# Performance work log

Measured on AMD Instinct MI355X. Metric: run time of the kernel, lower is better.

## Reference

```python
import jax, jax.numpy as jnp
import numpy as np

D_MODEL = 2048
NUM_HEADS = 16
D_K = D_MODEL // NUM_HEADS
LORA_R = 8
LORA_ALPHA = 16
SCALING = LORA_ALPHA / LORA_R  # 2.0
B, S = 2, 2048


def setup_inputs() -> dict:
    key = jax.random.key(0)
    ks = jax.random.split(key, 17)
    s = 1.0 / np.sqrt(D_MODEL)
    d = {"x": jax.random.normal(ks[0], (B, S, D_MODEL), jnp.float32)}
    i = 1
    for name in ("q", "k", "v", "o"):
        d[f"W{name}"] = jax.random.uniform(ks[i], (D_MODEL, D_MODEL), jnp.float32, -s, s); i += 1
        d[f"b{name}"] = jax.random.uniform(ks[i], (D_MODEL,), jnp.float32, -s, s); i += 1
        d[f"A{name}"] = jax.random.uniform(ks[i], (LORA_R, D_MODEL), jnp.float32, -s, s); i += 1
        # lora_B is zero-initialized in the module, but use small random so grads flow meaningfully
        d[f"B{name}"] = jax.random.normal(ks[i], (D_MODEL, LORA_R), jnp.float32) * 0.01; i += 1
    return d


def _lora_linear(x, W, b, A, Bm):
    # F.linear(x, W, b) + (x @ A.T @ B.T) * scaling
    return x @ W.T + b + ((x @ A.T) @ Bm.T) * SCALING


def reference(x, Wq, bq, Aq, Bq, Wk, bk, Ak, Bk, Wv, bv, Av, Bv, Wo, bo, Ao, Bo):
    batch = x.shape[0]
    q = _lora_linear(x, Wq, bq, Aq, Bq)
    k = _lora_linear(x, Wk, bk, Ak, Bk)
    v = _lora_linear(x, Wv, bv, Av, Bv)
    # [B, S, H, Dk] -> [B, H, S, Dk]
    q = q.reshape(batch, -1, NUM_HEADS, D_K).transpose(0, 2, 1, 3)
    k = k.reshape(batch, -1, NUM_HEADS, D_K).transpose(0, 2, 1, 3)
    v = v.reshape(batch, -1, NUM_HEADS, D_K).transpose(0, 2, 1, 3)
    scores = jnp.einsum("bhqd,bhkd->bhqk", q, k) / jnp.sqrt(jnp.float32(D_K))
    attn = jax.nn.softmax(scores, axis=-1)
    context = jnp.einsum("bhqk,bhkd->bhqd", attn, v)
    context = context.transpose(0, 2, 1, 3).reshape(batch, -1, D_MODEL)
    return _lora_linear(context, Wo, bo, Ao, Bo)
```

## Files before the change

kernel.cpp:

```cpp
#include <hip/hip_runtime.h>
#include <stdint.h>

typedef unsigned short u16;
typedef unsigned int   u32;
typedef __bf16  bf16x8 __attribute__((ext_vector_type(8)));
typedef float   f32x4  __attribute__((ext_vector_type(4)));

#define LORA_SCALE 2.0f
#define QSCALE 0.08838834764831845f
#define LOG2E  1.4426950408889634f
#define RESCALE_THR 8.0f

__device__ __forceinline__ u16 f2bf(float f){
  u32 u = __builtin_bit_cast(u32, f);
  u32 r = (u + 0x7fffu + ((u >> 16) & 1u)) >> 16;
  return (u16)r;
}
__device__ __forceinline__ float bf2f(u16 v){
  return __builtin_bit_cast(float, ((u32)v) << 16);
}
__device__ __forceinline__ u32 cvt_pk_bf16(float lo, float hi){
  u32 d;
  asm("v_cvt_pk_bf16_f32 %0, %1, %2" : "=v"(d) : "v"(lo), "v"(hi));
  return d;
}

typedef __attribute__((address_space(3))) u32 lds_u32_t;
typedef __attribute__((address_space(1))) const u32 g_u32_t;

__device__ __forceinline__ void gload16(const void* g, void* l){
  __builtin_amdgcn_global_load_lds((g_u32_t*)(unsigned long long)g,
                                   (lds_u32_t*)(u32)(unsigned long long)l,
                                   16, 0, 0);
}

__global__ __launch_bounds__(256) void cvt_w4(const float* __restrict__ W0,
    const float* __restrict__ W1, const float* __restrict__ W2,
    const float* __restrict__ W3, u16* __restrict__ wqkv, u16* __restrict__ wo){
  int sel = blockIdx.x >> 11;
  int inner = blockIdx.x & 2047;
  const float* src = sel==0 ? W0 : sel==1 ? W1 : sel==2 ? W2 : W3;
  u16* dst = sel<3 ? (wqkv + (size_t)sel*4194304) : wo;
  int i = (inner*256 + threadIdx.x) * 8;
  float4 a = *(const float4*)(src + i);
  float4 b = *(const float4*)(src + i + 4);
  u16 o[8] = {f2bf(a.x),f2bf(a.y),f2bf(a.z),f2bf(a.w),
              f2bf(b.x),f2bf(b.y),f2bf(b.z),f2bf(b.w)};
  *(uint4*)(dst + i) = *(const uint4*)o;
}

__global__ __launch_bounds__(256) void lora_x_fused(const float* __restrict__ x,
    const float* __restrict__ A0, const float* __restrict__ A1, const float* __restrict__ A2,
    float* __restrict__ xout, u16* __restrict__ xbf){
  int w = threadIdx.x >> 6, lane = threadIdx.x & 63;
  int m0 = blockIdx.x * 16 + w * 4;
  float acc[4][3][8];
  #pragma unroll
  for (int rr=0; rr<4; ++rr)
    #pragma unroll
    for (int g=0; g<3; ++g)
      #pragma unroll
      for (int r=0; r<8; ++r) acc[rr][g][r] = 0.f;
  const float* As[3] = {A0, A1, A2};
  #pragma unroll 1
  for (int it=0; it<8; ++it){
    int k = it*256 + lane*4;
    float4 xv[4];
    #pragma unroll
    for (int rr=0; rr<4; ++rr){
      xv[rr] = *(const float4*)(x + (size_t)(m0+rr)*2048 + k);
      u16 o[4] = {f2bf(xv[rr].x), f2bf(xv[rr].y), f2bf(xv[rr].z), f2bf(xv[rr].w)};
      *(uint2*)(xbf + (size_t)(m0+rr)*2048 + k) = *(const uint2*)o;
    }
    #pragma unroll
    for (int g=0; g<3; ++g){
      const float* Ag = As[g];
      #pragma unroll
      for (int r=0; r<8; ++r){
        float4 av = *(const float4*)(Ag + r*2048 + k);
        #pragma unroll
        for (int rr=0; rr<4; ++rr)
          acc[rr][g][r] += xv[rr].x*av.x + xv[rr].y*av.y + xv[rr].z*av.z + xv[rr].w*av.w;
      }
    }
  }
  #pragma unroll
  for (int rr=0; rr<4; ++rr)
    #pragma unroll
    for (int g=0; g<3; ++g)
      #pragma unroll
      for (int r=0; r<8; ++r){
        float v = acc[rr][g][r];
        #pragma unroll
        for (int off=32; off; off>>=1) v += __shfl_xor(v, off);
        if (lane == 0) xout[g*32768 + (m0+rr)*8 + r] = v;
      }
}

__global__ __launch_bounds__(256) void lora_xa_bf16(const u16* __restrict__ xin,
    const float* __restrict__ A0, float* __restrict__ xout){
  int w = threadIdx.x >> 6, lane = threadIdx.x & 63;
  int m0 = blockIdx.x * 16 + w * 4;
  float acc[4][8];
  #pragma unroll
  for (int rr=0; rr<4; ++rr)
    #pragma unroll
    for (int r=0; r<8; ++r) acc[rr][r] = 0.f;
  #pragma unroll 1
  for (int it=0; it<8; ++it){
    int k = it*256 + lane*4;
    float4 xv[4];
    #pragma unroll
    for (int rr=0; rr<4; ++rr){
      ushort4 u = *(const ushort4*)(xin + (size_t)(m0+rr)*2048 + k);
      xv[rr] = (float4){bf2f(u.x), bf2f(u.y), bf2f(u.z), bf2f(u.w)};
    }
    #pragma unroll
    for (int r=0; r<8; ++r){
      float4 av = *(const float4*)(A0 + r*2048 + k);
      #pragma unroll
      for (int rr=0; rr<4; ++rr)
        acc[rr][r] += xv[rr].x*av.x + xv[rr].y*av.y + xv[rr].z*av.z + xv[rr].w*av.w;
    }
  }
  #pragma unroll
  for (int rr=0; rr<4; ++rr)
    #pragma unroll
    for (int r=0; r<8; ++r){
      float v = acc[rr][r];
      #pragma unroll
      for (int off=32; off; off>>=1) v += __shfl_xor(v, off);
      if (lane == 0) xout[(m0+rr)*8 + r] = v;
    }
}

__device__ __forceinline__ void gemm_core_v7(
    const u16* __restrict__ Aptr,
    const u16* __restrict__ Wptr,
    u16* lds, int tid, f32x4 acc[8][4]){
  const int Kd = 2048;
  int l = tid & 63, w = tid >> 6;
  int l15 = l & 15, l4 = l >> 4;
  int wm = w >> 1, wn = w & 1;
  char* L = (char*)lds;
  int wb = w * 1024;
  const u16* asrc[4]; const u16* bsrc[2];
  #pragma unroll
  for (int i=0;i<4;i++){ int row=(i*4+w)*16+(l>>2); int sc=((l&3)^((row>>1)&3))<<3;
    asrc[i] = Aptr + (size_t)row*Kd + sc; }
  #pragma unroll
  for (int i=0;i<2;i++){ int row=(i*4+w)*16+(l>>2); int sc=((l&3)^((row>>1)&3))<<3;
    bsrc[i] = Wptr + (size_t)row*Kd + sc; }
  int aoff[8], boff[4];
  #pragma unroll
  for (int mr=0;mr<8;mr++){ int ra=wm*128+mr*16+l15; aoff[mr]=ra*64+((l4^((ra>>1)&3))<<4); }
  #pragma unroll
  for (int nr=0;nr<4;nr++){ int rb=wn*64+nr*16+l15; boff[nr]=16384+rb*64+((l4^((rb>>1)&3))<<4); }

  auto STG = [&](int kt, int sbase){
    char* D = L + sbase;
    gload16(asrc[0]+kt, D +        wb);
    gload16(asrc[1]+kt, D +  4096+ wb);
    gload16(asrc[2]+kt, D +  8192+ wb);
    gload16(asrc[3]+kt, D + 12288+ wb);
    gload16(bsrc[0]+kt, D + 16384+ wb);
    gload16(bsrc[1]+kt, D + 20480+ wb);
  };

  STG(0, 0); STG(32, 24576);
  asm volatile("s_waitcnt vmcnt(6)" ::: "memory");
  __builtin_amdgcn_s_barrier();

  int bb = 0, sb = 49152, kt2 = 64;
  #pragma unroll 1
  for (int t = 0; t < 64; ++t){
    bf16x8 af[4], bf[4];
    #pragma unroll
    for (int mr=0;mr<4;mr++) af[mr] = *(const bf16x8*)(L + bb + aoff[mr]);
    #pragma unroll
    for (int nr=0;nr<4;nr++) bf[nr] = *(const bf16x8*)(L + bb + boff[nr]);
    if (t < 62) STG(kt2, sb);
    __builtin_amdgcn_s_barrier();
    __builtin_amdgcn_s_setprio(1);
    #pragma unroll
    for (int mr=0;mr<4;mr++)
      #pragma unroll
      for (int nr=0;nr<4;nr++)
        acc[mr][nr] = __builtin_amdgcn_mfma_f32_16x16x32_bf16(af[mr], bf[nr], acc[mr][nr], 0,0,0);
    __builtin_amdgcn_s_setprio(0);
    __builtin_amdgcn_s_barrier();
    bf16x8 ag[4];
    #pragma unroll
    for (int mr=0;mr<4;mr++) ag[mr] = *(const bf16x8*)(L + bb + aoff[mr+4]);
    if (t < 62)       asm volatile("s_waitcnt vmcnt(6)" ::: "memory");
    else if (t == 62) asm volatile("s_waitcnt vmcnt(0)" ::: "memory");
    __builtin_amdgcn_s_barrier();
    __builtin_amdgcn_s_setprio(1);
    #pragma unroll
    for (int mr=0;mr<4;mr++)
      #pragma unroll
      for (int nr=0;nr<4;nr++)
        acc[mr+4][nr] = __builtin_amdgcn_mfma_f32_16x16x32_bf16(ag[mr], bf[nr], acc[mr+4][nr], 0,0,0);
    __builtin_amdgcn_s_setprio(0);
    __builtin_amdgcn_s_barrier();
    bb = (bb == 49152) ? 0 : bb + 24576;
    sb = (sb == 49152) ? 0 : sb + 24576;
    kt2 += 32;
  }
}

__global__ __launch_bounds__(256, 2) void gemm_qkv(
    const u16* __restrict__ A, const u16* __restrict__ W,
    const float* __restrict__ bq, const float* __restrict__ bk, const float* __restrict__ bv,
    const float* __restrict__ lBq, const float* __restrict__ lBk, const float* __restrict__ lBv,
    const float* __restrict__ xa, u16* __restrict__ Qb, u16* __restrict__ Kb, u16* __restrict__ Vtb){
  __shared__ u16 lds[36864];
  int tid = threadIdx.x;
  int l = tid & 63, w = tid >> 6;
  int l15 = l & 15, l4 = l >> 4;
  int wm = w >> 1, wn = w & 1;
  int bid = blockIdx.x;
  int xcd = bid & 7, local = bid >> 3;
  int mt = xcd*2 + (local >= 48);
  int nt = (local < 48) ? local : local - 48;
  int m0 = mt * 256, n0g = nt * 128;
  int which = nt >> 4;
  int n0 = (nt & 15) * 128;
  const float* bias = which==0 ? bq : which==1 ? bk : bv;
  const float* lB   = which==0 ? lBq : which==1 ? lBk : lBv;
  const float* xs   = xa + which*32768;

  f32x4 acc[8][4];
  #pragma unroll
  for (int mr=0; mr<8; mr++)
    #pragma unroll
    for (int nr=0; nr<4; nr++) acc[mr][nr] = (f32x4){0.f,0.f,0.f,0.f};

  gemm_core_v7(A + (size_t)m0*2048, W + (size_t)n0g*2048, lds, tid, acc);

  float bvv[4]; float4 lb0[4], lb1[4];
  #pragma unroll
  for (int nr=0; nr<4; nr++){
    int col = n0 + wn*64 + nr*16 + l15;
    bvv[nr] = bias[col];
    lb0[nr] = *(const float4*)(lB + col*8);
    lb1[nr] = *(const float4*)(lB + col*8 + 4);
  }

  if (which == 2){
    __syncthreads();
    char* L = (char*)lds;
    #pragma unroll
    for (int mr=0; mr<8; mr++){
      float vv[4][4];
      #pragma unroll
      for (int j=0; j<4; j++){
        int r = m0 + wm*128 + mr*16 + l4*4 + j;
        float4 xv0 = *(const float4*)(xs + (size_t)r*8);
        float4 xv1 = *(const float4*)(xs + (size_t)r*8 + 4);
        #pragma unroll
        for (int nr=0; nr<4; nr++)
          vv[nr][j] = acc[mr][nr][j] + bvv[nr] + LORA_SCALE * (
              xv0.x*lb0[nr].x + xv0.y*lb0[nr].y + xv0.z*lb0[nr].z + xv0.w*lb0[nr].w +
              xv1.x*lb1[nr].x + xv1.y*lb1[nr].y + xv1.z*lb1[nr].z + xv1.w*lb1[nr].w);
      }
      int s_ = wm*128 + mr*16 + l4*4;
      #pragma unroll
      for (int nr=0; nr<4; nr++){
        int d = wn*64 + nr*16 + l15;
        uint2 pk = {cvt_pk_bf16(vv[nr][0], vv[nr][1]), cvt_pk_bf16(vv[nr][2], vv[nr][3])};
        *(uint2*)(L + d*512 + ((s_*2) ^ ((d & 31) << 4))) = pk;
      }
    }
    __syncthreads();
    int bq_ = m0 >> 11, s0 = m0 & 2047, h = n0 >> 7;
    u16* vt = Vtb + ((size_t)((bq_*16 + h)*128)) * 2048;
    #pragma unroll
    for (int i=0; i<16; ++i){
      int flat = i*4096 + tid*16;
      int d = flat >> 9, s2 = flat & 511;
      uint4 val = *(const uint4*)(L + d*512 + (s2 ^ ((d & 31) << 4)));
      int sa = s0 + (s2 >> 1);
      *(uint4*)(vt + (size_t)d*2048 + (sa & ~63) + ((sa & 63) ^ ((d & 7) << 3))) = val;
    }
    return;
  }

  u16* outp = (which == 0) ? Qb : Kb;
  float oscale = (which == 0) ? QSCALE*LOG2E : 1.0f;
  #pragma unroll
  for (int mr=0; mr<8; mr++)
    #pragma unroll
    for (int j=0; j<4; j++){
      int r = m0 + wm*128 + mr*16 + l4*4 + j;
      float4 xv0 = *(const float4*)(xs + (size_t)r*8);
      float4 xv1 = *(const float4*)(xs + (size_t)r*8 + 4);
      #pragma unroll
      for (int nr=0; nr<4; nr++){
        int col = n0 + wn*64 + nr*16 + l15;
        float v = acc[mr][nr][j] + bvv[nr] + LORA_SCALE * (
            xv0.x*lb0[nr].x + xv0.y*lb0[nr].y + xv0.z*lb0[nr].z + xv0.w*lb0[nr].w +
            xv1.x*lb1[nr].x + xv1.y*lb1[nr].y + xv1.z*lb1[nr].z + xv1.w*lb1[nr].w);
        v *= oscale;
        int cs = col ^ ((r & 7) << 3);
        outp[(size_t)r*2048 + cs] = f2bf(v);
      }
    }
}

__global__ __launch_bounds__(256, 2) void gemm_o(
    const u16* __restrict__ A, const u16* __restrict__ W,
    const float* __restrict__ bias, const float* __restrict__ lB,
    const float* __restrict__ xa, float* __restrict__ outp){
  __shared__ u16 lds[36864];
  int tid = threadIdx.x;
  int l = tid & 63, w = tid >> 6;
  int l15 = l & 15, l4 = l >> 4;
  int wm = w >> 1, wn = w & 1;
  int bid = blockIdx.x;
  int xcd = bid & 7, local = bid >> 3;
  int mt = xcd*2 + (local >= 16);
  int nt = local & 15;
  int m0 = mt * 256, n0 = nt * 128;

  f32x4 acc[8][4];
  #pragma unroll
  for (int mr=0; mr<8; mr++)
    #pragma unroll
    for (int nr=0; nr<4; nr++) acc[mr][nr] = (f32x4){0.f,0.f,0.f,0.f};

  gemm_core_v7(A + (size_t)m0*2048, W + (size_t)n0*2048, lds, tid, acc);

  float bv[4]; float4 lb0[4], lb1[4];
  #pragma unroll
  for (int nr=0; nr<4; nr++){
    int col = n0 + wn*64 + nr*16 + l15;
    bv[nr] = bias[col];
    lb0[nr] = *(const float4*)(lB + col*8);
    lb1[nr] = *(const float4*)(lB + col*8 + 4);
  }
  #pragma unroll
  for (int mr=0; mr<8; mr++)
    #pragma unroll
    for (int j=0; j<4; j++){
      int r = m0 + wm*128 + mr*16 + l4*4 + j;
      float4 xv0 = *(const float4*)(xa + (size_t)r*8);
      float4 xv1 = *(const float4*)(xa + (size_t)r*8 + 4);
      #pragma unroll
      for (int nr=0; nr<4; nr++){
        int col = n0 + wn*64 + nr*16 + l15;
        float v = acc[mr][nr][j] + bv[nr] + LORA_SCALE * (
            xv0.x*lb0[nr].x + xv0.y*lb0[nr].y + xv0.z*lb0[nr].z + xv0.w*lb0[nr].w +
            xv1.x*lb1[nr].x + xv1.y*lb1[nr].y + xv1.z*lb1[nr].z + xv1.w*lb1[nr].w);
        outp[(size_t)r*2048 + col] = v;
      }
    }
}

__global__ __launch_bounds__(256, 2) void attn_kernel(
    const u16* __restrict__ Q, const u16* __restrict__ K,
    const u16* __restrict__ Vt, u16* __restrict__ ctx){
  __shared__ u16 buf[2][16384];
  __shared__ u16 Psh[4*32*64];
  int tid = threadIdx.x, w = tid >> 6, lane = tid & 63;
  int l15 = lane & 15, l4 = lane >> 4;
  int lin = blockIdx.x;
  int virt = (lin & 7) * 64 + (lin >> 3);
  int qt = virt & 15, bh = virt >> 4;
  int b = bh >> 4, h = bh & 15;
  const u16* Qg = Q + (size_t)(b*2048 + qt*128) * 2048 + h*128;
  const u16* Kg = K + (size_t)(b*2048) * 2048 + h*128;
  const u16* Vg = Vt + (size_t)bh * 128 * 2048;

  #pragma unroll
  for (int i=0; i<8; ++i){
    int e = (i*256 + tid) * 8;
    int r = e >> 7, cc = e & 127;
    gload16(Qg + (size_t)r*2048 + cc, (char*)buf[1] + i*4096 + w*1024);
  }
  #pragma unroll
  for (int i=0; i<4; ++i){
    int e = (i*256 + tid) * 8;
    int r = e >> 7, cc = e & 127;
    gload16(Kg + (size_t)r*2048 + cc, (char*)buf[0] + i*4096 + w*1024);
    int dd = e >> 6, c2 = e & 63;
    gload16(Vg + (size_t)dd*2048 + c2, (char*)buf[0] + 16384 + i*4096 + w*1024);
  }
  __syncthreads();

  bf16x8 qf[2][4];
  #pragma unroll
  for (int mi=0; mi<2; mi++){
    int r = w*32 + mi*16 + l15;
    #pragma unroll
    for (int kb=0; kb<4; kb++){
      int cc = (kb*32 + l4*8) ^ ((r & 7) << 3);
      qf[mi][kb] = *(const bf16x8*)(buf[1] + r*128 + cc);
    }
  }
  __syncthreads();

  f32x4 ctxa[2][8];
  #pragma unroll
  for (int mi=0; mi<2; mi++)
    #pragma unroll
    for (int nd=0; nd<8; nd++) ctxa[mi][nd] = (f32x4){0.f,0.f,0.f,0.f};
  float mrun[2] = {-3.0e38f, -3.0e38f};
  float lrun[2] = {0.f, 0.f};

  char* PwB = (char*)(Psh + w * (32*64));
  int psw = (l15 & 7) << 4;

  for (int t = 0; t < 32; ++t){
    int cur = t & 1;
    const u16* Kc = buf[cur];
    const u16* Vc = buf[cur] + 8192;
    if (t + 1 < 32){
      int kvn = (t + 1) * 64;
      char* bn = (char*)buf[cur ^ 1];
      #pragma unroll
      for (int i=0; i<4; ++i){
        int e = (i*256 + tid) * 8;
        int r = e >> 7, cc = e & 127;
        gload16(Kg + (size_t)(kvn + r)*2048 + cc, bn + i*4096 + w*1024);
        int dd = e >> 6, c2 = e & 63;
        gload16(Vg + (size_t)dd*2048 + kvn + c2, bn + 16384 + i*4096 + w*1024);
      }
    }
    f32x4 s[2][4];
    #pragma unroll
    for (int mi=0; mi<2; mi++)
      #pragma unroll
      for (int ni=0; ni<4; ni++) s[mi][ni] = (f32x4){0.f,0.f,0.f,0.f};
    __builtin_amdgcn_s_setprio(1);
    #pragma unroll
    for (int kb=0; kb<4; kb++){
      #pragma unroll
      for (int ni=0; ni<4; ni++){
        int r = ni*16 + l15;
        int cc = (kb*32 + l4*8) ^ ((r & 7) << 3);
        bf16x8 kf = *(const bf16x8*)(Kc + r*128 + cc);
        s[0][ni] = __builtin_amdgcn_mfma_f32_16x16x32_bf16(kf, qf[0][kb], s[0][ni], 0, 0, 0);
        s[1][ni] = __builtin_amdgcn_mfma_f32_16x16x32_bf16(kf, qf[1][kb], s[1][ni], 0, 0, 0);
      }
    }
    __builtin_amdgcn_s_setprio(0);
    float pm[2];
    #pragma unroll
    for (int mi=0; mi<2; mi++){
      float v = s[mi][0][0];
      #pragma unroll
      for (int ni=0; ni<4; ni++)
        #pragma unroll
        for (int j=0; j<4; j++) v = fmaxf(v, s[mi][ni][j]);
      v = fmaxf(v, __shfl_xor(v, 16));
      v = fmaxf(v, __shfl_xor(v, 32));
      pm[mi] = v;
    }
    bool need = (pm[0] > mrun[0] + RESCALE_THR) || (pm[1] > mrun[1] + RESCALE_THR);
    if (__any(need)){
      #pragma unroll
      for (int mi=0; mi<2; mi++){
        float mnew = fmaxf(mrun[mi], pm[mi]);
        float cr = exp2f(mrun[mi] - mnew);
        lrun[mi] *= cr;
        mrun[mi] = mnew;
        #pragma unroll
        for (int nd=0; nd<8; nd++) ctxa[mi][nd] *= cr;
      }
    }
    #pragma unroll
    for (int mi=0; mi<2; mi++){
      float ps = 0.f;
      #pragma unroll
      for (int ni=0; ni<4; ni++){
        float p0 = exp2f(s[mi][ni][0] - mrun[mi]);
        float p1 = exp2f(s[mi][ni][1] - mrun[mi]);
        float p2 = exp2f(s[mi][ni][2] - mrun[mi]);
        float p3 = exp2f(s[mi][ni][3] - mrun[mi]);
        ps += (p0 + p1) + (p2 + p3);
        uint2 pk = {cvt_pk_bf16(p0, p1), cvt_pk_bf16(p2, p3)};
        *(uint2*)(PwB + (mi*16 + l15)*128 + ((ni*32 + l4*8) ^ psw)) = pk;
      }
      ps += __shfl_xor(ps, 16);
      ps += __shfl_xor(ps, 32);
      lrun[mi] += ps;
    }
    bf16x8 pb[2][2];
    #pragma unroll
    for (int mi=0; mi<2; mi++)
      #pragma unroll
      for (int kvb=0; kvb<2; kvb++)
        pb[mi][kvb] = *(const bf16x8*)(PwB + (mi*16 + l15)*128 + ((kvb*64 + l4*16) ^ psw));
    __builtin_amdgcn_s_setprio(1);
    #pragma unroll
    for (int nd=0; nd<8; nd++){
      int dd = nd*16 + l15;
      int sw = (dd & 7) << 3;
      #pragma unroll
      for (int kvb=0; kvb<2; kvb++){
        bf16x8 vf = *(const bf16x8*)(Vc + dd*64 + ((kvb*32 + l4*8) ^ sw));
        ctxa[0][nd] = __builtin_amdgcn_mfma_f32_16x16x32_bf16(vf, pb[0][kvb], ctxa[0][nd], 0, 0, 0);
        ctxa[1][nd] = __builtin_amdgcn_mfma_f32_16x16x32_bf16(vf, pb[1][kvb], ctxa[1][nd], 0, 0, 0);
      }
    }
    __builtin_amdgcn_s_setprio(0);
    __syncthreads();
  }
  char* OwB = (char*)buf[0] + w*8192;
  #pragma unroll
  for (int mi=0; mi<2; mi++){
    float inv = 1.0f / lrun[mi];
    #pragma unroll
    for (int nd=0; nd<8; nd++){
      f32x4 c = ctxa[mi][nd] * inv;
      uint2 pk = {cvt_pk_bf16(c[0], c[1]), cvt_pk_bf16(c[2], c[3])};
      *(uint2*)(OwB + (mi*16 + l15)*256 + ((nd*32 + l4*8) ^ psw)) = pk;
    }
  }
  #pragma unroll
  for (int i=0; i<8; ++i){
    int row = i*4 + l4;
    int colb = l15*16;
    uint4 v = *(const uint4*)(OwB + row*256 + (colb ^ ((row & 7) << 4)));
    int srow = qt*128 + w*32 + row;
    *(uint4*)(ctx + ((size_t)(b*2048 + srow))*2048 + h*128 + colb/2) = v;
  }
}

extern "C" void kernel_launch(void* const* d_in, const int* in_sizes, int n_in,
                              void* d_out, int out_size, void* d_ws, size_t ws_size,
                              hipStream_t stream){
  const float* x  = (const float*)d_in[0];
  const float* Wq = (const float*)d_in[1];  const float* bq = (const float*)d_in[2];
  const float* Aq = (const float*)d_in[3];  const float* Bq = (const float*)d_in[4];
  const float* Wk = (const float*)d_in[5];  const float* bk = (const float*)d_in[6];
  const float* Ak = (const float*)d_in[7];  const float* Bk = (const float*)d_in[8];
  const float* Wv = (const float*)d_in[9];  const float* bv = (const float*)d_in[10];
  const float* Av = (const float*)d_in[11]; const float* Bv = (const float*)d_in[12];
  const float* Wo = (const float*)d_in[13]; const float* bo = (const float*)d_in[14];
  const float* Ao = (const float*)d_in[15]; const float* Bo = (const float*)d_in[16];

  char* ws = (char*)d_ws;
  size_t off = 0;
  u16* xbf  = (u16*)(ws + off); off += (size_t)4096*2048*2;
  u16* wqkv = (u16*)(ws + off); off += (size_t)3*2048*2048*2;
  u16* wob  = (u16*)(ws + off); off += (size_t)2048*2048*2;
  float* xa = (float*)(ws + off); off += (size_t)4*32768*4;
  u16* Qb  = (u16*)(ws + off); off += (size_t)4096*2048*2;
  u16* Kb  = (u16*)(ws + off); off += (size_t)4096*2048*2;
  u16* Vb  = (u16*)(ws + off); off += (size_t)4096*2048*2;
  u16* Vtb = (u16*)(ws + off); off += (size_t)4096*2048*2;
  if (ws_size < off) return;

  cvt_w4<<<8192, 256, 0, stream>>>(Wq, Wk, Wv, Wo, wqkv, wob);
  lora_x_fused<<<256, 256, 0, stream>>>(x, Aq, Ak, Av, xa, xbf);

  gemm_qkv<<<768, 256, 0, stream>>>(xbf, wqkv, bq, bk, bv, Bq, Bk, Bv, xa, Qb, Kb, Vtb);

  attn_kernel<<<512, 256, 0, stream>>>(Qb, Kb, Vtb, Vb);

  lora_xa_bf16<<<256, 256, 0, stream>>>(Vb, Ao, xa+98304);

  gemm_o<<<256, 256, 0, stream>>>(Vb, wob, bo, Bo, xa+98304, (float*)d_out);
}
```

Baseline: 363.3 us.

## Load GEMM A operand directly to registers, stage only B in LDS

The GEMM core now reads the A operand straight from global memory into registers, double-buffered across iterations, and stages only the B tile through a triple-buffered LDS ring. The main loop now has one barrier per k-step instead of four. LDS usage shrinks, which may let more blocks fit per CU. Separately, the LoRA down-projection kernels switch from four rows per wave to one row per wave and launch four times as many blocks for more parallelism. The risks are higher register pressure from the A buffers and uncoalesced global reads for A.

```diff
diff --git a/kernel.cpp b/kernel.cpp
--- a/kernel.cpp
+++ b/kernel.cpp
@@ -53,88 +53,88 @@
     const float* __restrict__ A0, const float* __restrict__ A1, const float* __restrict__ A2,
     float* __restrict__ xout, u16* __restrict__ xbf){
   int w = threadIdx.x >> 6, lane = threadIdx.x & 63;
-  int m0 = blockIdx.x * 16 + w * 4;
-  float acc[4][3][8];
-  #pragma unroll
-  for (int rr=0; rr<4; ++rr)
-    #pragma unroll
-    for (int g=0; g<3; ++g)
-      #pragma unroll
-      for (int r=0; r<8; ++r) acc[rr][g][r] = 0.f;
+  int m = blockIdx.x * 4 + w;
+  float acc[3][8];
+  #pragma unroll
+  for (int g=0; g<3; ++g)
+    #pragma unroll
+    for (int r=0; r<8; ++r) acc[g][r] = 0.f;
   const float* As[3] = {A0, A1, A2};
   #pragma unroll 1
   for (int it=0; it<8; ++it){
     int k = it*256 + lane*4;
-    float4 xv[4];
-    #pragma unroll
-    for (int rr=0; rr<4; ++rr){
-      xv[rr] = *(const float4*)(x + (size_t)(m0+rr)*2048 + k);
-      u16 o[4] = {f2bf(xv[rr].x), f2bf(xv[rr].y), f2bf(xv[rr].z), f2bf(xv[rr].w)};
-      *(uint2*)(xbf + (size_t)(m0+rr)*2048 + k) = *(const uint2*)o;
-    }
+    float4 xv = *(const float4*)(x + (size_t)m*2048 + k);
+    u16 o[4] = {f2bf(xv.x), f2bf(xv.y), f2bf(xv.z), f2bf(xv.w)};
+    *(uint2*)(xbf + (size_t)m*2048 + k) = *(const uint2*)o;
     #pragma unroll
     for (int g=0; g<3; ++g){
       const float* Ag = As[g];
       #pragma unroll
       for (int r=0; r<8; ++r){
         float4 av = *(const float4*)(Ag + r*2048 + k);
-        #pragma unroll
-        for (int rr=0; rr<4; ++rr)
-          acc[rr][g][r] += xv[rr].x*av.x + xv[rr].y*av.y + xv[rr].z*av.z + xv[rr].w*av.w;
-      }
-    }
-  }
-  #pragma unroll
-  for (int rr=0; rr<4; ++rr)
-    #pragma unroll
-    for (int g=0; g<3; ++g)
-      #pragma unroll
-      for (int r=0; r<8; ++r){
-        float v = acc[rr][g][r];
-        #pragma unroll
-        for (int off=32; off; off>>=1) v += __shfl_xor(v, off);
-        if (lane == 0) xout[g*32768 + (m0+rr)*8 + r] = v;
-      }
+        acc[g][r] += xv.x*av.x + xv.y*av.y + xv.z*av.z + xv.w*av.w;
+      }
+    }
+  }
+  #pragma unroll
+  for (int g=0; g<3; ++g)
+    #pragma unroll
+    for (int r=0; r<8; ++r){
+      float v = acc[g][r];
+      #pragma unroll
+      for (int off=32; off; off>>=1) v += __shfl_xor(v, off);
+      if (lane == 0) xout[g*32768 + m*8 + r] = v;
+    }
 }
 
 __global__ __launch_bounds__(256) void lora_xa_bf16(const u16* __restrict__ xin,
     const float* __restrict__ A0, float* __restrict__ xout){
   int w = threadIdx.x >> 6, lane = threadIdx.x & 63;
-  int m0 = blockIdx.x * 16 + w * 4;
-  float acc[4][8];
-  #pragma unroll
-  for (int rr=0; rr<4; ++rr)
-    #pragma unroll
-    for (int r=0; r<8; ++r) acc[rr][r] = 0.f;
+  int m = blockIdx.x * 4 + w;
+  float acc[8];
+  #pragma unroll
+  for (int r=0; r<8; ++r) acc[r] = 0.f;
   #pragma unroll 1
   for (int it=0; it<8; ++it){
     int k = it*256 + lane*4;
-    float4 xv[4];
-    #pragma unroll
-    for (int rr=0; rr<4; ++rr){
-      ushort4 u = *(const ushort4*)(xin + (size_t)(m0+rr)*2048 + k);
-      xv[rr] = (float4){bf2f(u.x), bf2f(u.y), bf2f(u.z), bf2f(u.w)};
-    }
+    ushort4 u = *(const ushort4*)(xin + (size_t)m*2048 + k);
+    float4 xv = {bf2f(u.x), bf2f(u.y), bf2f(u.z), bf2f(u.w)};
     #pragma unroll
     for (int r=0; r<8; ++r){
       float4 av = *(const float4*)(A0 + r*2048 + k);
-      #pragma unroll
-      for (int rr=0; rr<4; ++rr)
-        acc[rr][r] += xv[rr].x*av.x + xv[rr].y*av.y + xv[rr].z*av.z + xv[rr].w*av.w;
-    }
-  }
-  #pragma unroll
-  for (int rr=0; rr<4; ++rr)
-    #pragma unroll
-    for (int r=0; r<8; ++r){
-      float v = acc[rr][r];
-      #pragma unroll
-      for (int off=32; off; off>>=1) v += __shfl_xor(v, off);
-      if (lane == 0) xout[(m0+rr)*8 + r] = v;
-    }
-}
-
-__device__ __forceinline__ void gemm_core_v7(
+      acc[r] += xv.x*av.x + xv.y*av.y + xv.z*av.z + xv.w*av.w;
+    }
+  }
+  #pragma unroll
+  for (int r=0; r<8; ++r){
+    float v = acc[r];
+    #pragma unroll
+    for (int off=32; off; off>>=1) v += __shfl_xor(v, off);
+    if (lane == 0) xout[m*8 + r] = v;
+  }
+}
+
+#define STGB(T) { int bb_ = ((T)%3)*8192; \
+    gload16(bsrc0 + (T)*32, L + bb_ + wb); \
+    gload16(bsrc1 + (T)*32, L + bb_ + 4096 + wb); }
+
+#define GBODY(T, ACUR, ANEXT) { \
+  if ((T) < 63) { _Pragma("unroll") for (int mr=0;mr<8;mr++) \
+      ANEXT[mr] = *(const bf16x8*)(asrc[mr] + ((T)+1)*32); } \
+  if ((T) < 62) STGB((T)+2); \
+  const char* Bb = L + ((T)%3)*8192; \
+  bf16x8 bfr[4]; \
+  _Pragma("unroll") for (int nr=0;nr<4;nr++) bfr[nr] = *(const bf16x8*)(Bb + boff[nr]); \
+  __builtin_amdgcn_s_setprio(1); \
+  _Pragma("unroll") for (int mr=0;mr<8;mr++) \
+    _Pragma("unroll") for (int nr=0;nr<4;nr++) \
+      acc[mr][nr] = __builtin_amdgcn_mfma_f32_16x16x32_bf16(ACUR[mr], bfr[nr], acc[mr][nr], 0,0,0); \
+  __builtin_amdgcn_s_setprio(0); \
+  if ((T) < 62)       asm volatile("s_waitcnt vmcnt(10)" ::: "memory"); \
+  else if ((T) == 62) asm volatile("s_waitcnt vmcnt(8)"  ::: "memory"); \
+  __builtin_amdgcn_s_barrier(); }
+
+__device__ __forceinline__ void gemm_core_v9(
     const u16* __restrict__ Aptr,
     const u16* __restrict__ Wptr,
     u16* lds, int tid, f32x4 acc[8][4]){
@@ -144,68 +144,33 @@
   int wm = w >> 1, wn = w & 1;
   char* L = (char*)lds;
   int wb = w * 1024;
-  const u16* asrc[4]; const u16* bsrc[2];
-  #pragma unroll
-  for (int i=0;i<4;i++){ int row=(i*4+w)*16+(l>>2); int sc=((l&3)^((row>>1)&3))<<3;
-    asrc[i] = Aptr + (size_t)row*Kd + sc; }
-  #pragma unroll
-  for (int i=0;i<2;i++){ int row=(i*4+w)*16+(l>>2); int sc=((l&3)^((row>>1)&3))<<3;
-    bsrc[i] = Wptr + (size_t)row*Kd + sc; }
-  int aoff[8], boff[4];
-  #pragma unroll
-  for (int mr=0;mr<8;mr++){ int ra=wm*128+mr*16+l15; aoff[mr]=ra*64+((l4^((ra>>1)&3))<<4); }
-  #pragma unroll
-  for (int nr=0;nr<4;nr++){ int rb=wn*64+nr*16+l15; boff[nr]=16384+rb*64+((l4^((rb>>1)&3))<<4); }
-
-  auto STG = [&](int kt, int sbase){
-    char* D = L + sbase;
-    gload16(asrc[0]+kt, D +        wb);
-    gload16(asrc[1]+kt, D +  4096+ wb);
-    gload16(asrc[2]+kt, D +  8192+ wb);
-    gload16(asrc[3]+kt, D + 12288+ wb);
-    gload16(bsrc[0]+kt, D + 16384+ wb);
-    gload16(bsrc[1]+kt, D + 20480+ wb);
-  };
-
-  STG(0, 0); STG(32, 24576);
-  asm volatile("s_waitcnt vmcnt(6)" ::: "memory");
+  const u16* asrc[8];
+  #pragma unroll
+  for (int mr=0; mr<8; mr++)
+    asrc[mr] = Aptr + (size_t)(wm*128 + mr*16 + l15)*Kd + l4*8;
+  int i0 = tid,      r0 = i0>>2, g0 = (i0&3) ^ (r0&3);
+  int i1 = 256+tid,  r1 = i1>>2, g1 = (i1&3) ^ (r1&3);
+  const u16* bsrc0 = Wptr + (size_t)r0*Kd + g0*8;
+  const u16* bsrc1 = Wptr + (size_t)r1*Kd + g1*8;
+  int boff[4];
+  #pragma unroll
+  for (int nr=0;nr<4;nr++){
+    int rb = wn*64 + nr*16 + l15;
+    boff[nr] = rb*64 + ((l4 ^ (rb&3))<<4);
+  }
+
+  STGB(0); STGB(1);
+  bf16x8 aA[8], aB[8];
+  #pragma unroll
+  for (int mr=0;mr<8;mr++) aA[mr] = *(const bf16x8*)(asrc[mr]);
+  asm volatile("s_waitcnt vmcnt(10)" ::: "memory");
   __builtin_amdgcn_s_barrier();
 
-  int bb = 0, sb = 49152, kt2 = 64;
   #pragma unroll 1
-  for (int t = 0; t < 64; ++t){
-    bf16x8 af[4], bf[4];
-    #pragma unroll
-    for (int mr=0;mr<4;mr++) af[mr] = *(const bf16x8*)(L + bb + aoff[mr]);
-    #pragma unroll
-    for (int nr=0;nr<4;nr++) bf[nr] = *(const bf16x8*)(L + bb + boff[nr]);
-    if (t < 62) STG(kt2, sb);
-    __builtin_amdgcn_s_barrier();
-    __builtin_amdgcn_s_setprio(1);
-    #pragma unroll
-    for (int mr=0;mr<4;mr++)
-      #pragma unroll
-      for (int nr=0;nr<4;nr++)
-        acc[mr][nr] = __builtin_amdgcn_mfma_f32_16x16x32_bf16(af[mr], bf[nr], acc[mr][nr], 0,0,0);
-    __builtin_amdgcn_s_setprio(0);
-    __builtin_amdgcn_s_barrier();
-    bf16x8 ag[4];
-    #pragma unroll
-    for (int mr=0;mr<4;mr++) ag[mr] = *(const bf16x8*)(L + bb + aoff[mr+4]);
-    if (t < 62)       asm volatile("s_waitcnt vmcnt(6)" ::: "memory");
-    else if (t == 62) asm volatile("s_waitcnt vmcnt(0)" ::: "memory");
-    __builtin_amdgcn_s_barrier();
-    __builtin_amdgcn_s_setprio(1);
-    #pragma unroll
-    for (int mr=0;mr<4;mr++)
-      #pragma unroll
-      for (int nr=0;nr<4;nr++)
-        acc[mr+4][nr] = __builtin_amdgcn_mfma_f32_16x16x32_bf16(ag[mr], bf[nr], acc[mr+4][nr], 0,0,0);
-    __builtin_amdgcn_s_setprio(0);
-    __builtin_amdgcn_s_barrier();
-    bb = (bb == 49152) ? 0 : bb + 24576;
-    sb = (sb == 49152) ? 0 : sb + 24576;
-    kt2 += 32;
+  for (int t2 = 0; t2 < 32; ++t2){
+    int t = t2*2;
+    GBODY(t,   aA, aB);
+    GBODY(t+1, aB, aA);
   }
 }
 
@@ -214,7 +179,7 @@
     const float* __restrict__ bq, const float* __restrict__ bk, const float* __restrict__ bv,
     const float* __restrict__ lBq, const float* __restrict__ lBk, const float* __restrict__ lBv,
     const float* __restrict__ xa, u16* __restrict__ Qb, u16* __restrict__ Kb, u16* __restrict__ Vtb){
-  __shared__ u16 lds[36864];
+  __shared__ u16 lds[32768];
   int tid = threadIdx.x;
   int l = tid & 63, w = tid >> 6;
   int l15 = l & 15, l4 = l >> 4;
@@ -236,7 +201,7 @@
     #pragma unroll
     for (int nr=0; nr<4; nr++) acc[mr][nr] = (f32x4){0.f,0.f,0.f,0.f};
 
-  gemm_core_v7(A + (size_t)m0*2048, W + (size_t)n0g*2048, lds, tid, acc);
+  gemm_core_v9(A + (size_t)m0*2048, W + (size_t)n0g*2048, lds, tid, acc);
 
   float bvv[4]; float4 lb0[4], lb1[4];
   #pragma unroll
@@ -312,7 +277,7 @@
     const u16* __restrict__ A, const u16* __restrict__ W,
     const float* __restrict__ bias, const float* __restrict__ lB,
     const float* __restrict__ xa, float* __restrict__ outp){
-  __shared__ u16 lds[36864];
+  __shared__ u16 lds[12288];
   int tid = threadIdx.x;
   int l = tid & 63, w = tid >> 6;
   int l15 = l & 15, l4 = l >> 4;
@@ -329,7 +294,7 @@
     #pragma unroll
     for (int nr=0; nr<4; nr++) acc[mr][nr] = (f32x4){0.f,0.f,0.f,0.f};
 
-  gemm_core_v7(A + (size_t)m0*2048, W + (size_t)n0*2048, lds, tid, acc);
+  gemm_core_v9(A + (size_t)m0*2048, W + (size_t)n0*2048, lds, tid, acc);
 
   float bv[4]; float4 lb0[4], lb1[4];
   #pragma unroll
@@ -554,13 +519,13 @@
   if (ws_size < off) return;
 
   cvt_w4<<<8192, 256, 0, stream>>>(Wq, Wk, Wv, Wo, wqkv, wob);
-  lora_x_fused<<<256, 256, 0, stream>>>(x, Aq, Ak, Av, xa, xbf);
+  lora_x_fused<<<1024, 256, 0, stream>>>(x, Aq, Ak, Av, xa, xbf);
 
   gemm_qkv<<<768, 256, 0, stream>>>(xbf, wqkv, bq, bk, bv, Bq, Bk, Bv, xa, Qb, Kb, Vtb);
 
   attn_kernel<<<512, 256, 0, stream>>>(Qb, Kb, Vtb, Vb);
 
-  lora_xa_bf16<<<256, 256, 0, stream>>>(Vb, Ao, xa+98304);
+  lora_xa_bf16<<<1024, 256, 0, stream>>>(Vb, Ao, xa+98304);
 
   gemm_o<<<256, 256, 0, stream>>>(Vb, wob, bo, Bo, xa+98304, (float*)d_out);
 }
```

After: 476.8 us. 31.2% more time.
